# Optimization experiments

Measured on AMD Instinct MI355X. Metric: run time of the kernel, lower is better.

## Reference

```python
import jax, jax.numpy as jnp
import numpy as np

N_NODE, N_NET, E = 100000, 20000, 200000
H_NODE, H_NET, H_PIN = 64, 32, 16
O_NODE, O_NET = 32, 64


def setup_inputs() -> dict:
    key = jax.random.key(0)
    ks = jax.random.split(key, 8)
    return {
        'node_feat': jax.random.normal(ks[0], (N_NODE, H_NODE), jnp.float32),
        'net_feat': jax.random.normal(ks[1], (N_NET, H_NET), jnp.float32),
        'pin_feat': jax.random.normal(ks[2], (E, H_PIN), jnp.float32),
        'edge_node': jax.random.randint(ks[3], (E,), 0, N_NODE, jnp.int32),
        'edge_net': jax.random.randint(ks[4], (E,), 0, N_NET, jnp.int32),
        'W1': jax.random.normal(ks[5], (H_NODE, O_NET), jnp.float32) * 0.05,
        'b1': jnp.zeros((O_NET,), jnp.float32),
        'W2': jax.random.normal(ks[6], (H_PIN, H_NET * O_NODE), jnp.float32) * 0.05,
        'b2': jnp.zeros((H_NET * O_NODE,), jnp.float32),
        'b_nn': jnp.zeros((O_NODE,), jnp.float32),
    }


def reference(node_feat, net_feat, pin_feat, edge_node, edge_net, W1, b1, W2, b2, b_nn):
    ones = jnp.ones((E,), node_feat.dtype)
    # ---- relation 'pins': node -> net, DGL GraphConv with norm='both' ----
    out_deg = jnp.clip(jax.ops.segment_sum(ones, edge_node, num_segments=N_NODE), 1.0)  # src out-degree
    in_deg = jnp.clip(jax.ops.segment_sum(ones, edge_net, num_segments=N_NET), 1.0)     # dst in-degree
    src = node_feat * jax.lax.rsqrt(out_deg)[:, None]                                   # [N_node, H_node]
    agg = jax.ops.segment_sum(src[edge_node], edge_net, num_segments=N_NET)             # [N_net, H_node]
    net_out = (agg * jax.lax.rsqrt(in_deg)[:, None]) @ W1 + b1                           # [N_net, O_net]
    # ---- relation 'pinned': net -> node, DGL NNConv (mean aggregator) ----
    We = (pin_feat @ W2 + b2).reshape(E, H_NET, O_NODE)                                  # per-edge weight matrix
    msg = jnp.einsum('ei,eio->eo', net_feat[edge_net], We)                               # [E, O_node]
    node_deg = jnp.clip(jax.ops.segment_sum(ones, edge_node, num_segments=N_NODE), 1.0)
    node_out = jax.ops.segment_sum(msg, edge_node, num_segments=N_NODE) / node_deg[:, None] + b_nn
    return node_out, net_out
```

## Files before the change

### kernel.cpp

```cpp
#include <hip/hip_runtime.h>
#include <hip/hip_bf16.h>

#define N_NODE 100000
#define N_NET  20000
#define NE     200000
#define H_NODE 64
#define H_NET  32
#define H_PIN  16
#define O_NODE 32
#define O_NET  64
#define CSR_STRIDE 64


#define OFF_NETCNT  400000
#define OFF_CSR     480000
#define OFF_Z       10720000
#define OFF_C       31200000
#define ZERO_BYTES  480000

static __device__ __forceinline__ unsigned short f2bf(float f) {
    unsigned int u = __float_as_uint(f);
    u += 0x7fff + ((u >> 16) & 1);
    return (unsigned short)(u >> 16);
}
static __device__ __forceinline__ float bf2f(unsigned short h) {
    return __uint_as_float(((unsigned int)h) << 16);
}

#define BLD_EDGE_BLKS 782
#define BLD_Z_BLKS    1250
#define BLD_INIT_BLKS 3125
#define ZNPB 16

__global__ void k_build(const int* __restrict__ en, const int* __restrict__ em,
                        int* __restrict__ node_deg, int* __restrict__ net_cnt,
                        int2* __restrict__ csr,
                        const float* __restrict__ net_feat,
                        const float* __restrict__ W2, const float* __restrict__ b2,
                        unsigned short* __restrict__ Zb, float* __restrict__ C,
                        const float* __restrict__ b_nn,
                        float* __restrict__ out_node) {
    int t = threadIdx.x, b = blockIdx.x;
    if (b < BLD_EDGE_BLKS) {
        int e = b * 256 + t;
        if (e < NE) {
            int v = en[e], n = em[e];
            atomicAdd(&node_deg[v], 1);
            int slot = atomicAdd(&net_cnt[n], 1);
            if (slot < CSR_STRIDE) csr[n * CSR_STRIDE + slot] = make_int2(e, v);
        }
        return;
    }
    if (b < BLD_EDGE_BLKS + BLD_Z_BLKS) {
        __shared__ float sy[ZNPB][H_NET];
        int base = (b - BLD_EDGE_BLKS) * ZNPB;
        for (int idx = t; idx < ZNPB * H_NET; idx += 256)
            sy[idx >> 5][idx & 31] = net_feat[(base + (idx >> 5)) * H_NET + (idx & 31)];
        __syncthreads();
        int o = t & 31, k4 = (t >> 5) & 3, rep = t >> 7;
        const float* w2p = W2 + (k4 * 4) * 1024 + o;
        float4 acc[8];
#pragma unroll
        for (int g = 0; g < 8; g++) acc[g] = make_float4(0.f, 0.f, 0.f, 0.f);
#pragma unroll 4
        for (int i = 0; i < H_NET; i++) {
            float w0 = w2p[0 * 1024 + i * 32];
            float w1 = w2p[1 * 1024 + i * 32];
            float w2v = w2p[2 * 1024 + i * 32];
            float w3 = w2p[3 * 1024 + i * 32];
#pragma unroll
            for (int g = 0; g < 8; g++) {
                float y = sy[rep * 8 + g][i];
                acc[g].x += w0 * y; acc[g].y += w1 * y;
                acc[g].z += w2v * y; acc[g].w += w3 * y;
            }
        }
#pragma unroll
        for (int g = 0; g < 8; g++) {
            int n = base + rep * 8 + g;
            ushort4 uz;
            uz.x = f2bf(acc[g].x); uz.y = f2bf(acc[g].y);
            uz.z = f2bf(acc[g].z); uz.w = f2bf(acc[g].w);
            *(ushort4*)&Zb[(size_t)n * 512 + o * 16 + k4 * 4] = uz;
        }
#pragma unroll
        for (int r = 0; r < 2; r++) {
            int idx = t + r * 256;
            int g = idx >> 5, oo = idx & 31;
            float a = 0.f;
#pragma unroll
            for (int i = 0; i < H_NET; i++) a += sy[g][i] * b2[i * 32 + oo];
            C[(base + g) * 32 + oo] = a;
        }
        return;
    }
    int idx = (b - BLD_EDGE_BLKS - BLD_Z_BLKS) * 256 + t;
    ((float4*)out_node)[idx] = ((const float4*)b_nn)[idx & 7];
}

__global__ void k_net(const float* __restrict__ node_feat,
                      const int* __restrict__ node_deg,
                      const int* __restrict__ net_cnt,
                      const int2* __restrict__ csr,
                      const float* __restrict__ W1,
                      const float* __restrict__ b1,
                      const unsigned short* __restrict__ Zb,
                      const float* __restrict__ Cg,
                      const float* __restrict__ pin_feat,
                      float* __restrict__ out_net, float* __restrict__ out_node) {
    __shared__ float  spin[4][32][16];
    __shared__ float4 srow4[4][16];
    int t = threadIdx.x;
    int w = t >> 6, l = t & 63;
    int n = blockIdx.x * 4 + w;
    int beg = n * CSR_STRIDE, deg = net_cnt[n];
    int o = l & 31;
    int half = l >> 5;
    int q = l >> 4, f = l & 15;

    float z[16];
    {
        const uint4* zp = (const uint4*)&Zb[(size_t)n * 512 + o * 16];
        uint4 za = zp[0], zb = zp[1];
        unsigned int uu[8] = {za.x, za.y, za.z, za.w, zb.x, zb.y, zb.z, zb.w};
#pragma unroll
        for (int i = 0; i < 8; i++) {
            z[2 * i]     = bf2f((unsigned short)(uu[i] & 0xffffu));
            z[2 * i + 1] = bf2f((unsigned short)(uu[i] >> 16));
        }
    }
    float c = Cg[n * 32 + o];

    const float4* nf4 = (const float4*)node_feat;
    const float4* pf4 = (const float4*)pin_feat;

    float4 acc4 = make_float4(0.f, 0.f, 0.f, 0.f);

    for (int j0 = 0; j0 < deg; j0 += 32) {
        int cnt = deg - j0; if (cnt > 32) cnt = 32;
        int vj = 0, ej = 0; float sj = 0.f;
        if (l < cnt) {
            int2 ev = csr[beg + j0 + l];
            ej = ev.x; vj = ev.y;
            float dv = (float)node_deg[vj]; if (dv < 1.f) dv = 1.f;
            sj = rsqrtf(dv);
        }
        {
            int jj = l >> 2;
            int src = (jj < cnt) ? jj : cnt - 1;
            int e = __shfl(ej, src);
            float4 pv = pf4[(size_t)e * 4 + (l & 3)];
            ((float4*)&spin[w][jj][0])[l & 3] = pv;
        }
        if (cnt > 16) {
            int jj = 16 + (l >> 2);
            int src = (jj < cnt) ? jj : cnt - 1;
            int e = __shfl(ej, src);
            float4 pv = pf4[(size_t)e * 4 + (l & 3)];
            ((float4*)&spin[w][jj][0])[l & 3] = pv;
        }
        {
            int vv[4]; float ss[4];
#pragma unroll
            for (int r = 0; r < 4; r++) {
                int jj = r * 4 + q;
                int src = (jj < cnt) ? jj : cnt - 1;
                vv[r] = __shfl(vj, src);
                float sv = __shfl(sj, src);
                ss[r] = (jj < cnt) ? sv : 0.f;
            }
            float4 xx[4];
#pragma unroll
            for (int r = 0; r < 4; r++) xx[r] = nf4[(size_t)vv[r] * 16 + f];
#pragma unroll
            for (int r = 0; r < 4; r++) {
                acc4.x += xx[r].x * ss[r]; acc4.y += xx[r].y * ss[r];
                acc4.z += xx[r].z * ss[r]; acc4.w += xx[r].w * ss[r];
            }
        }
        if (cnt > 16) {
            int vv[4]; float ss[4];
#pragma unroll
            for (int r = 0; r < 4; r++) {
                int jj = 16 + r * 4 + q;
                int src = (jj < cnt) ? jj : cnt - 1;
                vv[r] = __shfl(vj, src);
                float sv = __shfl(sj, src);
                ss[r] = (jj < cnt) ? sv : 0.f;
            }
            float4 xx[4];
#pragma unroll
            for (int r = 0; r < 4; r++) xx[r] = nf4[(size_t)vv[r] * 16 + f];
#pragma unroll
            for (int r = 0; r < 4; r++) {
                acc4.x += xx[r].x * ss[r]; acc4.y += xx[r].y * ss[r];
                acc4.z += xx[r].z * ss[r]; acc4.w += xx[r].w * ss[r];
            }
        }
        for (int jj = 0; jj < cnt; jj += 2) {
            int je = jj + half;
            int src = (je < cnt) ? je : cnt - 1;
            int v = __shfl(vj, src);
            float sv = __shfl(sj, src);
            float inv = sv * sv;
            const float4* pr = (const float4*)&spin[w][src][0];
            float m = c;
#pragma unroll
            for (int k4 = 0; k4 < 4; k4++) {
                float4 pv = pr[k4];
                m += pv.x * z[k4 * 4 + 0] + pv.y * z[k4 * 4 + 1]
                   + pv.z * z[k4 * 4 + 2] + pv.w * z[k4 * 4 + 3];
            }
            if (je < cnt) atomicAdd(&out_node[(size_t)v * O_NODE + o], m * inv);
        }
    }
    acc4.x += __shfl_xor(acc4.x, 16); acc4.y += __shfl_xor(acc4.y, 16);
    acc4.z += __shfl_xor(acc4.z, 16); acc4.w += __shfl_xor(acc4.w, 16);
    acc4.x += __shfl_xor(acc4.x, 32); acc4.y += __shfl_xor(acc4.y, 32);
    acc4.z += __shfl_xor(acc4.z, 32); acc4.w += __shfl_xor(acc4.w, 32);
    float dn = (deg < 1) ? 1.f : (float)deg;
    float rs = rsqrtf(dn);
    if (l < 16)
        srow4[w][l] = make_float4(acc4.x * rs, acc4.y * rs, acc4.z * rs, acc4.w * rs);
    __syncthreads();
    {
        const float* a = (const float*)&srow4[w][0];
        float oacc = b1[l];
#pragma unroll 16
        for (int h = 0; h < H_NODE; h++) oacc += a[h] * W1[h * O_NET + l];
        out_net[n * O_NET + l] = oacc;
    }
}

extern "C" void kernel_launch(void* const* d_in, const int* in_sizes, int n_in,
                              void* d_out, int out_size, void* d_ws, size_t ws_size,
                              hipStream_t stream) {
    const float* node_feat = (const float*)d_in[0];
    const float* net_feat  = (const float*)d_in[1];
    const float* pin_feat  = (const float*)d_in[2];
    const int*   edge_node = (const int*)d_in[3];
    const int*   edge_net  = (const int*)d_in[4];
    const float* W1        = (const float*)d_in[5];
    const float* b1        = (const float*)d_in[6];
    const float* W2        = (const float*)d_in[7];
    const float* b2        = (const float*)d_in[8];
    const float* b_nn      = (const float*)d_in[9];

    float* out_node = (float*)d_out;
    float* out_net  = out_node + (size_t)N_NODE * O_NODE;

    char* ws = (char*)d_ws;
    int*            node_deg = (int*)ws;
    int*            net_cnt  = (int*)(ws + OFF_NETCNT);
    int2*           csr      = (int2*)(ws + OFF_CSR);
    unsigned short* Zb       = (unsigned short*)(ws + OFF_Z);
    float*          C        = (float*)(ws + OFF_C);

    (void)hipMemsetAsync(ws, 0, ZERO_BYTES, stream);

    k_build<<<BLD_EDGE_BLKS + BLD_Z_BLKS + BLD_INIT_BLKS, 256, 0, stream>>>(
        edge_node, edge_net, node_deg, net_cnt, csr,
        net_feat, W2, b2, Zb, C, b_nn, out_node);

    k_net<<<N_NET / 4, 256, 0, stream>>>(
        node_feat, node_deg, net_cnt, csr,
        W1, b1, Zb, C, pin_feat, out_net, out_node);
}
```

Baseline: 162.7 us.

## Replace scattered node atomics with per-edge message buffer and node-side gather kernel

```diff
diff --git a/kernel.cpp b/kernel.cpp
--- a/kernel.cpp
+++ b/kernel.cpp
@@ -9,13 +9,16 @@
 #define H_PIN  16
 #define O_NODE 32
 #define O_NET  64
-#define CSR_STRIDE 64
+#define CSR_STRIDE  64
+#define NODE_STRIDE 16
 
 
 #define OFF_NETCNT  400000
 #define OFF_CSR     480000
-#define OFF_Z       10720000
-#define OFF_C       31200000
+#define OFF_NCSR    10720000
+#define OFF_Z       17120000
+#define OFF_C       37600000
+#define OFF_MSG     40160000
 #define ZERO_BYTES  480000
 
 static __device__ __forceinline__ unsigned short f2bf(float f) {
@@ -29,29 +32,27 @@
 
 #define BLD_EDGE_BLKS 782
 #define BLD_Z_BLKS    1250
-#define BLD_INIT_BLKS 3125
 #define ZNPB 16
 
 __global__ void k_build(const int* __restrict__ en, const int* __restrict__ em,
                         int* __restrict__ node_deg, int* __restrict__ net_cnt,
-                        int2* __restrict__ csr,
+                        int2* __restrict__ csr, int* __restrict__ node_csr,
                         const float* __restrict__ net_feat,
                         const float* __restrict__ W2, const float* __restrict__ b2,
-                        unsigned short* __restrict__ Zb, float* __restrict__ C,
-                        const float* __restrict__ b_nn,
-                        float* __restrict__ out_node) {
+                        unsigned short* __restrict__ Zb, float* __restrict__ C) {
     int t = threadIdx.x, b = blockIdx.x;
     if (b < BLD_EDGE_BLKS) {
         int e = b * 256 + t;
         if (e < NE) {
             int v = en[e], n = em[e];
-            atomicAdd(&node_deg[v], 1);
+            int ns = atomicAdd(&node_deg[v], 1);
+            if (ns < NODE_STRIDE) node_csr[v * NODE_STRIDE + ns] = e;
             int slot = atomicAdd(&net_cnt[n], 1);
             if (slot < CSR_STRIDE) csr[n * CSR_STRIDE + slot] = make_int2(e, v);
         }
         return;
     }
-    if (b < BLD_EDGE_BLKS + BLD_Z_BLKS) {
+    {
         __shared__ float sy[ZNPB][H_NET];
         int base = (b - BLD_EDGE_BLKS) * ZNPB;
         for (int idx = t; idx < ZNPB * H_NET; idx += 256)
@@ -92,10 +93,7 @@
             for (int i = 0; i < H_NET; i++) a += sy[g][i] * b2[i * 32 + oo];
             C[(base + g) * 32 + oo] = a;
         }
-        return;
-    }
-    int idx = (b - BLD_EDGE_BLKS - BLD_Z_BLKS) * 256 + t;
-    ((float4*)out_node)[idx] = ((const float4*)b_nn)[idx & 7];
+    }
 }
 
 __global__ void k_net(const float* __restrict__ node_feat,
@@ -107,7 +105,7 @@
                       const unsigned short* __restrict__ Zb,
                       const float* __restrict__ Cg,
                       const float* __restrict__ pin_feat,
-                      float* __restrict__ out_net, float* __restrict__ out_node) {
+                      float* __restrict__ out_net, float* __restrict__ msg) {
     __shared__ float  spin[4][32][16];
     __shared__ float4 srow4[4][16];
     int t = threadIdx.x;
@@ -200,9 +198,7 @@
         for (int jj = 0; jj < cnt; jj += 2) {
             int je = jj + half;
             int src = (je < cnt) ? je : cnt - 1;
-            int v = __shfl(vj, src);
-            float sv = __shfl(sj, src);
-            float inv = sv * sv;
+            int e = __shfl(ej, src);
             const float4* pr = (const float4*)&spin[w][src][0];
             float m = c;
 #pragma unroll
@@ -211,7 +207,7 @@
                 m += pv.x * z[k4 * 4 + 0] + pv.y * z[k4 * 4 + 1]
                    + pv.z * z[k4 * 4 + 2] + pv.w * z[k4 * 4 + 3];
             }
-            if (je < cnt) atomicAdd(&out_node[(size_t)v * O_NODE + o], m * inv);
+            if (je < cnt) msg[(size_t)e * O_NODE + o] = m;
         }
     }
     acc4.x += __shfl_xor(acc4.x, 16); acc4.y += __shfl_xor(acc4.y, 16);
@@ -232,6 +228,32 @@
     }
 }
 
+__global__ void k_node(const int* __restrict__ node_deg,
+                       const int* __restrict__ node_csr,
+                       const float* __restrict__ msg,
+                       const float* __restrict__ b_nn,
+                       float* __restrict__ out_node) {
+    int t = threadIdx.x;
+    int w = t >> 6, l = t & 63;
+    int h = l >> 5, o = l & 31;
+    int v = blockIdx.x * 8 + w * 2 + h;
+    int dg = node_deg[v];
+    int eid = node_csr[v * NODE_STRIDE + (l & 15)];
+    int dother = __shfl(dg, l ^ 32);
+    int jmax = dg > dother ? dg : dother;
+    if (jmax > NODE_STRIDE) jmax = NODE_STRIDE;
+    float acc = 0.f;
+    for (int j = 0; j < jmax; ++j) {
+        int jc = (j < dg) ? j : 0;
+        int e = __shfl(eid, (l & 32) + jc);
+        e = (dg > 0) ? e : 0;
+        float m = msg[(size_t)e * O_NODE + o];
+        acc += (j < dg) ? m : 0.f;
+    }
+    float r = 1.f / fmaxf((float)dg, 1.f);
+    out_node[(size_t)v * O_NODE + o] = b_nn[o] + acc * r;
+}
+
 extern "C" void kernel_launch(void* const* d_in, const int* in_sizes, int n_in,
                               void* d_out, int out_size, void* d_ws, size_t ws_size,
                               hipStream_t stream) {
@@ -253,16 +275,21 @@
     int*            node_deg = (int*)ws;
     int*            net_cnt  = (int*)(ws + OFF_NETCNT);
     int2*           csr      = (int2*)(ws + OFF_CSR);
+    int*            node_csr = (int*)(ws + OFF_NCSR);
     unsigned short* Zb       = (unsigned short*)(ws + OFF_Z);
     float*          C        = (float*)(ws + OFF_C);
+    float*          msg      = (float*)(ws + OFF_MSG);
 
     (void)hipMemsetAsync(ws, 0, ZERO_BYTES, stream);
 
-    k_build<<<BLD_EDGE_BLKS + BLD_Z_BLKS + BLD_INIT_BLKS, 256, 0, stream>>>(
-        edge_node, edge_net, node_deg, net_cnt, csr,
-        net_feat, W2, b2, Zb, C, b_nn, out_node);
+    k_build<<<BLD_EDGE_BLKS + BLD_Z_BLKS, 256, 0, stream>>>(
+        edge_node, edge_net, node_deg, net_cnt, csr, node_csr,
+        net_feat, W2, b2, Zb, C);
 
     k_net<<<N_NET / 4, 256, 0, stream>>>(
         node_feat, node_deg, net_cnt, csr,
-        W1, b1, Zb, C, pin_feat, out_net, out_node);
-}
+        W1, b1, Zb, C, pin_feat, out_net, msg);
+
+    k_node<<<N_NODE / 8, 256, 0, stream>>>(
+        node_deg, node_csr, msg, b_nn, out_node);
+}
```

Result: slower. 174.0 us (+7.0%).
